# Kernel optimization log

Hardware: AMD Instinct MI355X
Metric: run time of the kernel (lower is better)

Reference implementation:

```python
import jax, jax.numpy as jnp
import numpy as np

B, T, D, H, E, R, M, HID, NB = 8, 832, 1024, 16, 16, 8, 16, 4096, 576
LORA_SCALE = 1.0 / R  # alpha / rank


def _ln(x, g, b, eps=1e-6):
    m = x.mean(-1, keepdims=True)
    v = ((x - m) ** 2).mean(-1, keepdims=True)
    return (x - m) / jnp.sqrt(v + eps) * g + b


def setup_inputs() -> dict:
    key = jax.random.key(0)
    ks = jax.random.split(key, 12)
    sd = 0.02
    return {
        's': jax.random.normal(ks[0], (B, T, D), jnp.float32),
        'attn_mask': jnp.zeros((1, 1, T, T), jnp.float32),
        'g1': jnp.ones((D,), jnp.float32),
        'b1': jnp.zeros((D,), jnp.float32),
        'w_qkv': jax.random.normal(ks[1], (D, 3 * D), jnp.float32) * sd,
        'b_qkv': jnp.zeros((3 * D,), jnp.float32),
        'w_proj': jax.random.normal(ks[2], (D, D), jnp.float32) * sd,
        'b_proj': jnp.zeros((D,), jnp.float32),
        'g2': jnp.ones((D,), jnp.float32),
        'b2': jnp.zeros((D,), jnp.float32),
        'w_fc1': jax.random.normal(ks[3], (D, HID), jnp.float32) * sd,
        'b_fc1': jnp.zeros((HID,), jnp.float32),
        'w_fc2': jax.random.normal(ks[4], (HID, D), jnp.float32) * sd,
        'b_fc2': jnp.zeros((D,), jnp.float32),
        'lora_A': jax.random.normal(ks[5], (E, D, R), jnp.float32) * sd,
        'lora_B': jax.random.normal(ks[6], (E, R, D), jnp.float32) * sd,
        'active_expert_indices': jnp.arange(E, dtype=jnp.int32),
        'num_backbone_tokens': NB,
    }


def reference(s, attn_mask, g1, b1, w_qkv, b_qkv, w_proj, b_proj,
              g2, b2, w_fc1, b_fc1, w_fc2, b_fc2, lora_A, lora_B,
              active_expert_indices, num_backbone_tokens):
    Bb, Tt, Dd = s.shape
    hd = Dd // H
    # --- shared attention ---
    x = _ln(s, g1, b1)
    qkv = (x @ w_qkv + b_qkv).reshape(Bb, Tt, 3, H, hd).transpose(2, 0, 3, 1, 4)
    q, k, v = qkv[0], qkv[1], qkv[2]  # [B,H,T,hd]
    scores = jnp.einsum('bhqd,bhkd->bhqk', q * (hd ** -0.5), k) + attn_mask
    p = jax.nn.softmax(scores, axis=-1)
    o = jnp.einsum('bhqk,bhkd->bhqd', p, v).transpose(0, 2, 1, 3).reshape(Bb, Tt, Dd)
    s = s + (o @ w_proj + b_proj)
    # --- shared MLP ---
    s_norm = _ln(s, g2, b2)
    shared = jax.nn.gelu(s_norm @ w_fc1 + b_fc1, approximate=False) @ w_fc2 + b_fc2
    # --- per-expert LoRA on expert token segment ---
    nb = num_backbone_tokens
    z = s_norm[:, nb:, :].reshape(Bb, -1, M, Dd)  # [B,K,M,D]
    Ak = lora_A[active_expert_indices]            # [K,D,R]
    Bk = lora_B[active_expert_indices]            # [K,R,D]
    down = jnp.einsum('bkmd,kdr->bkmr', z, Ak)
    up = jnp.einsum('bkmr,krd->bkmd', down, Bk) * LORA_SCALE
    shared = shared.at[:, nb:, :].add(up.reshape(Bb, -1, Dd))
    return s + shared
```

## Files before the change

### kernel.cpp

```cpp
#include <hip/hip_runtime.h>
#include <hip/hip_bf16.h>
#include <math.h>

typedef unsigned short u16;
typedef __attribute__((ext_vector_type(8))) short short8;
typedef __attribute__((ext_vector_type(4))) float f32x4;

constexpr int B_ = 8, T_ = 832, D_ = 1024, H_ = 16, HID_ = 4096, NB_ = 576;
constexpr int NT_ = B_ * T_;

__device__ inline u16 f2b(float f) {
    union { float f; unsigned u; } x{f};
    unsigned r = (x.u + 0x7FFFu + ((x.u >> 16) & 1u)) >> 16;
    return (u16)r;
}
__device__ inline float b2f(u16 b) {
    union { unsigned u; float f; } x; x.u = ((unsigned)b) << 16; return x.f;
}

__device__ inline float erf_inl(float x) {
    float ax = fabsf(x);
    float t = __frcp_rn(1.0f + 0.3275911f * ax);
    float p = 1.061405429f;
    p = p * t - 1.453152027f;
    p = p * t + 1.421413741f;
    p = p * t - 0.284496736f;
    p = p * t + 0.254829592f;
    p = p * t;
    float e = 1.0f - p * __expf(-ax * ax);
    return copysignf(e, x);
}

__device__ inline void gload_lds16(const void* g, void* l) {
    __builtin_amdgcn_global_load_lds((const __attribute__((address_space(1))) void*)g,
                                     (__attribute__((address_space(3))) void*)l, 16, 0, 0);
}

__global__ __launch_bounds__(256) void wtrans_kernel(const float* __restrict__ in,
                                                     u16* __restrict__ out, int K, int N) {
    __shared__ u16 tile[32][34];
    int n0 = blockIdx.x * 32, k0 = blockIdx.y * 32;
    int tx = threadIdx.x & 31, ty = threadIdx.x >> 5;
    for (int i = 0; i < 4; i++) {
        int k = k0 + ty + i * 8;
        tile[ty + i * 8][tx] = f2b(in[(size_t)k * N + n0 + tx]);
    }
    __syncthreads();
    for (int i = 0; i < 4; i++) {
        int n = n0 + ty + i * 8;
        out[(size_t)n * K + k0 + tx] = tile[tx][ty + i * 8];
    }
}

__global__ __launch_bounds__(256) void ln_kernel(const float* __restrict__ x,
                                                 const float* __restrict__ g,
                                                 const float* __restrict__ bt,
                                                 u16* __restrict__ out) {
    int row = blockIdx.x, tid = threadIdx.x;
    float4 v = ((const float4*)(x + (size_t)row * D_))[tid];
    float s = v.x + v.y + v.z + v.w;
    float q = v.x * v.x + v.y * v.y + v.z * v.z + v.w * v.w;
    for (int o = 1; o < 64; o <<= 1) { s += __shfl_xor(s, o); q += __shfl_xor(q, o); }
    __shared__ float red[4][2];
    if ((tid & 63) == 0) { red[tid >> 6][0] = s; red[tid >> 6][1] = q; }
    __syncthreads();
    s = red[0][0] + red[1][0] + red[2][0] + red[3][0];
    q = red[0][1] + red[1][1] + red[2][1] + red[3][1];
    float mean = s * (1.0f / D_);
    float var = q * (1.0f / D_) - mean * mean;
    float inv = rsqrtf(fmaxf(var, 0.f) + 1e-6f);
    float4 gv = ((const float4*)g)[tid];
    float4 bv = ((const float4*)bt)[tid];
    u16* orow = out + (size_t)row * D_ + tid * 4;
    orow[0] = f2b((v.x - mean) * inv * gv.x + bv.x);
    orow[1] = f2b((v.y - mean) * inv * gv.y + bv.y);
    orow[2] = f2b((v.z - mean) * inv * gv.z + bv.z);
    orow[3] = f2b((v.w - mean) * inv * gv.w + bv.w);
}

template<int BM, int BN, int WR, int WC, int MODE>
__global__ __launch_bounds__(WR * WC * 64, (WR * WC == 8) ? 2 : 3)
void gemm3(const u16* __restrict__ A, const u16* __restrict__ Bt,
           const float* __restrict__ bias, const float* __restrict__ resid,
           void* __restrict__ outp, int M, int N, int K) {
    constexpr int THREADS = WR * WC * 64;
    constexpr int MF = BM / WR / 16;
    constexpr int NF = BN / WC / 16;
    constexpr int NROWS = BM + BN;
    constexpr int CHUNKS = NROWS * 4 / THREADS;
    constexpr int LDSU = NROWS * 32;
    __shared__ u16 lds_[3 * LDSU];

    int tid = threadIdx.x, l = tid & 63, w = tid >> 6;
    int lrow = l & 15, lgrp = l >> 4;
    int wr = w / WC, wc = w % WC;

    int nwg = gridDim.x * gridDim.y;
    int bid = blockIdx.y * gridDim.x + blockIdx.x;
    int cpx = nwg >> 3;
    int swz = (bid & 7) * cpx + (bid >> 3);
    int bx = swz % gridDim.x, by = swz / gridDim.x;
    int m0 = by * BM, n0 = bx * BN;

    const u16* src[CHUNKS];
    int ldst[CHUNKS];
    for (int i = 0; i < CHUNKS; i++) {
        int c = i * THREADS + tid;
        int lc = (c & ~7) | ((c ^ (c >> 3)) & 7);
        int row = lc >> 2, colu = (lc & 3) * 8;
        src[i] = (row < BM) ? A + (size_t)(m0 + row) * K + colu
                            : Bt + (size_t)(n0 + row - BM) * K + colu;
        ldst[i] = c * 8;
    }

#define STAGE3(bufi, kt)                                                    \
    do {                                                                    \
        int kof = (kt) * 32;                                                \
        u16* bb = lds_ + (bufi) * LDSU;                                     \
        for (int i = 0; i < CHUNKS; i++) gload_lds16(src[i] + kof, bb + ldst[i]); \
    } while (0)

    f32x4 acc[MF][NF];
    for (int m = 0; m < MF; m++) for (int n = 0; n < NF; n++) acc[m][n] = (f32x4){0, 0, 0, 0};

    int aidx[MF], bidx[NF];
    for (int m = 0; m < MF; m++) {
        int row = wr * 64 + m * 16 + lrow;
        aidx[m] = (row * 32 + lgrp * 8) ^ (((row >> 1) & 7) << 3);
    }
    for (int n = 0; n < NF; n++) {
        int row = BM + wc * 64 + n * 16 + lrow;
        bidx[n] = (row * 32 + lgrp * 8) ^ (((row >> 1) & 7) << 3);
    }

    int nkt = K >> 5;
    STAGE3(0, 0);
    STAGE3(1, 1);
    if constexpr (CHUNKS == 3) asm volatile("s_waitcnt vmcnt(3)" ::: "memory");
    else                       asm volatile("s_waitcnt vmcnt(4)" ::: "memory");
    asm volatile("s_barrier" ::: "memory");

    int cur = 0;
    for (int t = 0; t < nkt; ++t) {
        int sb = cur + 2; if (sb >= 3) sb -= 3;
        if (t + 2 < nkt) STAGE3(sb, t + 2);

        const u16* bp = lds_ + cur * LDSU;
        short8 af[MF], bfr[NF];
        for (int m = 0; m < MF; m++) af[m] = *(const short8*)(bp + aidx[m]);
        for (int n = 0; n < NF; n++) bfr[n] = *(const short8*)(bp + bidx[n]);

        __builtin_amdgcn_s_setprio(1);
        for (int m = 0; m < MF; m++)
            for (int n = 0; n < NF; n++)
                acc[m][n] = __builtin_amdgcn_mfma_f32_16x16x32_bf16(af[m], bfr[n], acc[m][n], 0, 0, 0);
        __builtin_amdgcn_s_setprio(0);

        if (t + 2 < nkt) {
            if constexpr (CHUNKS == 3) asm volatile("s_waitcnt vmcnt(3)" ::: "memory");
            else                       asm volatile("s_waitcnt vmcnt(4)" ::: "memory");
        } else if (t + 1 < nkt) {
            asm volatile("s_waitcnt vmcnt(0)" ::: "memory");
        }
        asm volatile("s_barrier" ::: "memory");
        cur = cur + 1; if (cur == 3) cur = 0;
    }
#undef STAGE3

    for (int m = 0; m < MF; m++) {
        int rbase = m0 + wr * 64 + m * 16 + lgrp * 4;
        for (int n = 0; n < NF; n++) {
            int col = n0 + wc * 64 + n * 16 + lrow;
            float bv = bias[col];
            for (int j = 0; j < 4; j++) {
                int row = rbase + j;
                float v = acc[m][n][j] + bv;
                size_t off = (size_t)row * N + col;
                if constexpr (MODE == 0) {
                    ((u16*)outp)[off] = f2b(v);
                } else if constexpr (MODE == 1) {
                    ((float*)outp)[off] = v + resid[off];
                } else {
                    float gl = 0.5f * v * (1.0f + erf_inl(v * 0.70710678118654752f));
                    ((u16*)outp)[off] = f2b(gl);
                }
            }
        }
    }
}

__global__ __launch_bounds__(256) void vtrans_kernel(const u16* __restrict__ qkv,
                                                     u16* __restrict__ vt) {
    __shared__ u16 tile[32][66];
    int bh = blockIdx.y, b = bh >> 4, h = bh & 15;
    int t0 = blockIdx.x * 32;
    int dx = threadIdx.x & 63, ty = threadIdx.x >> 6;
    for (int i = 0; i < 8; i++) {
        int tt = ty * 8 + i;
        tile[tt][dx] = qkv[(size_t)(b * T_ + t0 + tt) * 3072 + 2048 + h * 64 + dx];
    }
    __syncthreads();
    int tx = threadIdx.x & 31, dy = threadIdx.x >> 5;
    for (int i = 0; i < 8; i++) {
        int d = dy * 8 + i;
        vt[((size_t)bh * 64 + d) * T_ + t0 + tx] = tile[tx][d];
    }
}

__global__ __launch_bounds__(512, 4) void attn_kernel(const u16* __restrict__ qkv,
                                                      const u16* __restrict__ vt,
                                                      const float* __restrict__ mask,
                                                      u16* __restrict__ obuf) {
    __shared__ u16 Ks[2][4096];
    __shared__ u16 Vs[2][4096];
    __shared__ u16 Ps[8][1024];
    int qt = blockIdx.x, bh = blockIdx.y, b = bh >> 4, h = bh & 15;
    int tid = threadIdx.x, w = tid >> 6, l = tid & 63;
    int lrow = l & 15, lgrp = l >> 4;

    int qrow = qt * 128 + w * 16 + lrow;
    int qrc = qrow < T_ ? qrow : T_ - 1;
    const u16* qp = qkv + (size_t)(b * T_ + qrc) * 3072 + h * 64 + lgrp * 8;
    short8 aq0, aq1;
    {
        short8 r0 = *(const short8*)qp;
        short8 r1 = *(const short8*)(qp + 32);
        for (int i = 0; i < 8; i++) {
            aq0[i] = (short)f2b(b2f((u16)r0[i]) * 0.125f);
            aq1[i] = (short)f2b(b2f((u16)r1[i]) * 0.125f);
        }
    }

    int tq0 = qt * 128 + w * 16 + lgrp * 4;
    bool qvalid = tq0 < T_;
    const float* mrowp[4];
#pragma unroll
    for (int j = 0; j < 4; j++) {
        int tq = tq0 + j; if (tq >= T_) tq = T_ - 1;
        mrowp[j] = mask + (size_t)tq * T_;
    }

    float m_r[4], l_r[4];
    f32x4 oacc[4];
    for (int j = 0; j < 4; j++) { m_r[j] = -1e30f; l_r[j] = 0.f; }
    for (int n = 0; n < 4; n++) oacc[n] = (f32x4){0, 0, 0, 0};

    int srow = tid >> 3, sp = tid & 7;
    int se = (sp ^ (srow & 7)) * 8;
    const u16* kbase = qkv + (size_t)b * T_ * 3072 + 1024 + h * 64;
    const u16* vbase = vt + (size_t)bh * 64 * T_;

#define STAGE_KV(buf, kk0)                                                        \
    do {                                                                          \
        gload_lds16(kbase + (size_t)((kk0) + srow) * 3072 + se, &Ks[buf][w * 512]); \
        gload_lds16(vbase + (size_t)srow * T_ + (kk0) + se, &Vs[buf][w * 512]);     \
    } while (0)

    float mc[16], mn[16];
    STAGE_KV(0, 0);
#pragma unroll
    for (int j = 0; j < 4; j++)
#pragma unroll
        for (int c = 0; c < 4; c++)
            mc[j * 4 + c] = mrowp[j][c * 16 + lrow];
    __syncthreads();

    int cur = 0;
    u16* Pw = Ps[w];
    int swl = lrow & 7;
    int slot0 = (lgrp ^ swl) * 8, slot1 = ((lgrp + 4) ^ swl) * 8;

    for (int kt = 0; kt < 13; ++kt) {
        int kk0 = kt * 64;
        if (kt < 12) {
            STAGE_KV(cur ^ 1, kk0 + 64);
#pragma unroll
            for (int j = 0; j < 4; j++)
#pragma unroll
                for (int c = 0; c < 4; c++)
                    mn[j * 4 + c] = mrowp[j][kk0 + 64 + c * 16 + lrow];
        }

        f32x4 sc[4];
        for (int c = 0; c < 4; c++) sc[c] = (f32x4){0, 0, 0, 0};
        const u16* Kb = Ks[cur];
        __builtin_amdgcn_s_setprio(1);
        for (int c = 0; c < 4; c++) {
            const u16* krow = Kb + (c * 16 + lrow) * 64;
            short8 bk0 = *(const short8*)(krow + slot0);
            short8 bk1 = *(const short8*)(krow + slot1);
            sc[c] = __builtin_amdgcn_mfma_f32_16x16x32_bf16(aq0, bk0, sc[c], 0, 0, 0);
            sc[c] = __builtin_amdgcn_mfma_f32_16x16x32_bf16(aq1, bk1, sc[c], 0, 0, 0);
        }
        __builtin_amdgcn_s_setprio(0);

        int lo3 = lrow & 7, hi = lrow >> 3;
#pragma unroll
        for (int j = 0; j < 4; j++) {
            float s0 = sc[0][j] + mc[j * 4 + 0];
            float s1 = sc[1][j] + mc[j * 4 + 1];
            float s2 = sc[2][j] + mc[j * 4 + 2];
            float s3 = sc[3][j] + mc[j * 4 + 3];
            float mx = fmaxf(fmaxf(s0, s1), fmaxf(s2, s3));
            mx = fmaxf(mx, __shfl_xor(mx, 1));
            mx = fmaxf(mx, __shfl_xor(mx, 2));
            mx = fmaxf(mx, __shfl_xor(mx, 4));
            mx = fmaxf(mx, __shfl_xor(mx, 8));
            float mnew = fmaxf(m_r[j], mx);
            float scf = __expf(m_r[j] - mnew);
            float p0 = __expf(s0 - mnew), p1 = __expf(s1 - mnew);
            float p2 = __expf(s2 - mnew), p3 = __expf(s3 - mnew);
            float ps = (p0 + p1) + (p2 + p3);
            ps += __shfl_xor(ps, 1); ps += __shfl_xor(ps, 2);
            ps += __shfl_xor(ps, 4); ps += __shfl_xor(ps, 8);
            l_r[j] = l_r[j] * scf + ps;
            m_r[j] = mnew;
            for (int n = 0; n < 4; n++) oacc[n][j] *= scf;
            int row_p = lgrp * 4 + j, swp = row_p & 7;
            u16* pr = Pw + row_p * 64;
            pr[((hi ^ swp) * 8) + lo3]       = f2b(p0);
            pr[(((2 + hi) ^ swp) * 8) + lo3] = f2b(p1);
            pr[(((4 + hi) ^ swp) * 8) + lo3] = f2b(p2);
            pr[(((6 + hi) ^ swp) * 8) + lo3] = f2b(p3);
        }

        short8 ap0 = *(const short8*)&Pw[lrow * 64 + slot0];
        short8 ap1 = *(const short8*)&Pw[lrow * 64 + slot1];
        const u16* Vb = Vs[cur];
        __builtin_amdgcn_s_setprio(1);
        for (int n = 0; n < 4; n++) {
            const u16* vrow = Vb + (n * 16 + lrow) * 64;
            short8 bv0 = *(const short8*)(vrow + slot0);
            short8 bv1 = *(const short8*)(vrow + slot1);
            oacc[n] = __builtin_amdgcn_mfma_f32_16x16x32_bf16(ap0, bv0, oacc[n], 0, 0, 0);
            oacc[n] = __builtin_amdgcn_mfma_f32_16x16x32_bf16(ap1, bv1, oacc[n], 0, 0, 0);
        }
        __builtin_amdgcn_s_setprio(0);

        __syncthreads();
#pragma unroll
        for (int i = 0; i < 16; i++) mc[i] = mn[i];
        cur ^= 1;
    }
#undef STAGE_KV

    if (qvalid) {
        for (int j = 0; j < 4; j++) {
            float inv = 1.0f / l_r[j];
            int t = tq0 + j;
            for (int n = 0; n < 4; n++)
                obuf[(size_t)(b * T_ + t) * 1024 + h * 64 + n * 16 + lrow] = f2b(oacc[n][j] * inv);
        }
    }
}

__global__ __launch_bounds__(256) void lora_kernel(const u16* __restrict__ snorm,
                                                   const float* __restrict__ lA,
                                                   const float* __restrict__ lB,
                                                   const int* __restrict__ idx,
                                                   float* __restrict__ outp) {
    __shared__ float down[16][8];
    int blk = blockIdx.x, b = blk >> 4, kk = blk & 15;
    int e = idx[kk];
    int tok0 = b * T_ + NB_ + kk * 16;
    int tid = threadIdx.x;
    if (tid < 128) {
        int m = tid >> 3, r = tid & 7;
        const u16* z = snorm + (size_t)(tok0 + m) * D_;
        const float* Ae = lA + (size_t)e * D_ * 8 + r;
        float acc = 0.f;
        for (int d = 0; d < D_; ++d) acc += b2f(z[d]) * Ae[(size_t)d * 8];
        down[m][r] = acc;
    }
    __syncthreads();
    for (int ci = 0; ci < 4; ci++) {
        int col = tid + ci * 256;
        float br[8];
        for (int r = 0; r < 8; r++) br[r] = lB[((size_t)e * 8 + r) * D_ + col];
        for (int m = 0; m < 16; m++) {
            float acc = 0.f;
            for (int r = 0; r < 8; r++) acc += down[m][r] * br[r];
            outp[(size_t)(tok0 + m) * D_ + col] += acc * 0.125f;
        }
    }
}

extern "C" void kernel_launch(void* const* d_in, const int* in_sizes, int n_in,
                              void* d_out, int out_size, void* d_ws, size_t ws_size,
                              hipStream_t stream) {
    const float* s      = (const float*)d_in[0];
    const float* mask   = (const float*)d_in[1];
    const float* g1     = (const float*)d_in[2];
    const float* b1     = (const float*)d_in[3];
    const float* w_qkv  = (const float*)d_in[4];
    const float* b_qkv  = (const float*)d_in[5];
    const float* w_proj = (const float*)d_in[6];
    const float* b_proj = (const float*)d_in[7];
    const float* g2     = (const float*)d_in[8];
    const float* b2     = (const float*)d_in[9];
    const float* w_fc1  = (const float*)d_in[10];
    const float* b_fc1  = (const float*)d_in[11];
    const float* w_fc2  = (const float*)d_in[12];
    const float* b_fc2  = (const float*)d_in[13];
    const float* lA     = (const float*)d_in[14];
    const float* lB     = (const float*)d_in[15];
    const int*   eidx   = (const int*)d_in[16];
    float* out = (float*)d_out;
    char* ws = (char*)d_ws;

    u16*   wqkvT = (u16*)(ws + 0);
    u16*   wprojT= (u16*)(ws + 6291456);
    u16*   wfc1T = (u16*)(ws + 8388608);
    u16*   wfc2T = (u16*)(ws + 16777216);
    float* s1    = (float*)(ws + 25165824);
    u16*   xln   = (u16*)(ws + 52428800);
    u16*   vt    = (u16*)(ws + 66060288);
    u16*   qkv   = (u16*)(ws + 79691776);
    u16*   h     = (u16*)(ws + 66060288);

    wtrans_kernel<<<dim3(3072 / 32, 1024 / 32), 256, 0, stream>>>(w_qkv, wqkvT, 1024, 3072);
    wtrans_kernel<<<dim3(1024 / 32, 1024 / 32), 256, 0, stream>>>(w_proj, wprojT, 1024, 1024);
    wtrans_kernel<<<dim3(4096 / 32, 1024 / 32), 256, 0, stream>>>(w_fc1, wfc1T, 1024, 4096);
    wtrans_kernel<<<dim3(1024 / 32, 4096 / 32), 256, 0, stream>>>(w_fc2, wfc2T, 4096, 1024);

    ln_kernel<<<NT_, 256, 0, stream>>>(s, g1, b1, xln);
    gemm3<128, 256, 2, 4, 0><<<dim3(3072 / 256, NT_ / 128), 512, 0, stream>>>(xln, wqkvT, b_qkv, nullptr, qkv, NT_, 3072, 1024);
    vtrans_kernel<<<dim3(26, 128), 256, 0, stream>>>(qkv, vt);
    attn_kernel<<<dim3(7, 128), 512, 0, stream>>>(qkv, vt, mask, xln);
    gemm3<128, 128, 2, 2, 1><<<dim3(1024 / 128, NT_ / 128), 256, 0, stream>>>(xln, wprojT, b_proj, s, s1, NT_, 1024, 1024);
    ln_kernel<<<NT_, 256, 0, stream>>>(s1, g2, b2, xln);
    gemm3<128, 256, 2, 4, 2><<<dim3(4096 / 256, NT_ / 128), 512, 0, stream>>>(xln, wfc1T, b_fc1, nullptr, h, NT_, 4096, 1024);
    gemm3<128, 128, 2, 2, 1><<<dim3(1024 / 128, NT_ / 128), 256, 0, stream>>>(h, wfc2T, b_fc2, s1, out, NT_, 1024, 4096);
    lora_kernel<<<128, 256, 0, stream>>>(xln, lA, lB, eidx, out);
}
```

Baseline: 431.3 us.

## Add 256x256 double-buffered GEMM kernel for QKV and FC1 projections

Introduces a new gemm4 kernel with 256x256 output tiles, 8 waves each computing 128x64, two LDS buffers with XOR-swizzled direct global-to-LDS loads, XCD-aware block swizzling and MFMA priority hints. It replaces the triple-buffered 128x256 gemm3 for the QKV and FC1 GEMMs. The larger tile is meant to raise arithmetic intensity and cut redundant global loads. In exchange each thread holds 128 accumulator registers, there are fewer workgroups (312 for QKV), and there is less pipelining depth.

```diff
diff --git a/kernel.cpp b/kernel.cpp
--- a/kernel.cpp
+++ b/kernel.cpp
@@ -76,6 +76,103 @@
     orow[1] = f2b((v.y - mean) * inv * gv.y + bv.y);
     orow[2] = f2b((v.z - mean) * inv * gv.z + bv.z);
     orow[3] = f2b((v.w - mean) * inv * gv.w + bv.w);
+}
+
+template<int MODE>
+__global__ __launch_bounds__(512, 2)
+void gemm4(const u16* __restrict__ A, const u16* __restrict__ Bt,
+           const float* __restrict__ bias, void* __restrict__ outp,
+           int M, int N, int K) {
+    __shared__ u16 lds4[2][16384];
+    int tid = threadIdx.x, l = tid & 63, w = tid >> 6;
+    int lrow = l & 15, lgrp = l >> 4;
+    int wr = w >> 2, wc = w & 3;
+
+    int nwg = gridDim.x * gridDim.y;
+    int bid = blockIdx.y * gridDim.x + blockIdx.x;
+    int cpx = nwg >> 3;
+    int swz = (bid & 7) * cpx + (bid >> 3);
+    int bx = swz % gridDim.x, by = swz / gridDim.x;
+    int m0 = by * 256, n0 = bx * 256;
+
+    const u16* src[4];
+    int ldst[4];
+    for (int i = 0; i < 2; i++) {
+        int c = i * 512 + tid;
+        int row = c >> 2, s = c & 3;
+        int col = (s ^ (row & 3)) * 8;
+        src[i]     = A  + (size_t)(m0 + row) * K + col;
+        ldst[i]    = c * 8;
+        src[i + 2] = Bt + (size_t)(n0 + row) * K + col;
+        ldst[i + 2] = 8192 + c * 8;
+    }
+
+#define STAGE4(cb, t)                                                       \
+    do {                                                                    \
+        u16* bb = &lds4[cb][0];                                             \
+        int ko = (t) * 32;                                                  \
+        for (int i = 0; i < 4; i++) gload_lds16(src[i] + ko, bb + ldst[i]); \
+    } while (0)
+
+    f32x4 acc[8][4];
+    for (int m = 0; m < 8; m++) for (int n = 0; n < 4; n++) acc[m][n] = (f32x4){0, 0, 0, 0};
+
+    int sl = (lgrp ^ (lrow & 3)) * 8;
+    int aidx[8], bidx[4];
+    for (int m = 0; m < 8; m++) {
+        int row = wr * 128 + (m >> 2) * 64 + (m & 3) * 16 + lrow;
+        aidx[m] = row * 32 + sl;
+    }
+    for (int n = 0; n < 4; n++) {
+        int row = wc * 64 + n * 16 + lrow;
+        bidx[n] = 8192 + row * 32 + sl;
+    }
+
+    int nkt = K >> 5;
+    STAGE4(0, 0);
+    asm volatile("s_waitcnt vmcnt(0)" ::: "memory");
+    asm volatile("s_barrier" ::: "memory");
+
+    for (int t = 0; t < nkt; ++t) {
+        int cb = t & 1;
+        if (t + 1 < nkt) STAGE4(cb ^ 1, t + 1);
+        const u16* bp = &lds4[cb][0];
+        short8 bf[4];
+        for (int n = 0; n < 4; n++) bf[n] = *(const short8*)(bp + bidx[n]);
+        for (int hm = 0; hm < 2; hm++) {
+            short8 af[4];
+            for (int mi = 0; mi < 4; mi++) af[mi] = *(const short8*)(bp + aidx[hm * 4 + mi]);
+            __builtin_amdgcn_s_setprio(1);
+            for (int mi = 0; mi < 4; mi++)
+                for (int n = 0; n < 4; n++)
+                    acc[hm * 4 + mi][n] =
+                        __builtin_amdgcn_mfma_f32_16x16x32_bf16(af[mi], bf[n], acc[hm * 4 + mi][n], 0, 0, 0);
+            __builtin_amdgcn_s_setprio(0);
+        }
+        if (t + 1 < nkt) {
+            asm volatile("s_waitcnt vmcnt(0)" ::: "memory");
+            asm volatile("s_barrier" ::: "memory");
+        }
+    }
+#undef STAGE4
+
+    for (int m = 0; m < 8; m++) {
+        int rbase = m0 + wr * 128 + (m >> 2) * 64 + (m & 3) * 16 + lgrp * 4;
+        for (int n = 0; n < 4; n++) {
+            int col = n0 + wc * 64 + n * 16 + lrow;
+            float bv = bias[col];
+            for (int j = 0; j < 4; j++) {
+                float v = acc[m][n][j] + bv;
+                size_t off = (size_t)(rbase + j) * N + col;
+                if constexpr (MODE == 0) {
+                    ((u16*)outp)[off] = f2b(v);
+                } else {
+                    float gl = 0.5f * v * (1.0f + erf_inl(v * 0.70710678118654752f));
+                    ((u16*)outp)[off] = f2b(gl);
+                }
+            }
+        }
+    }
 }
 
 template<int BM, int BN, int WR, int WC, int MODE>
@@ -424,12 +521,12 @@
     wtrans_kernel<<<dim3(1024 / 32, 4096 / 32), 256, 0, stream>>>(w_fc2, wfc2T, 4096, 1024);
 
     ln_kernel<<<NT_, 256, 0, stream>>>(s, g1, b1, xln);
-    gemm3<128, 256, 2, 4, 0><<<dim3(3072 / 256, NT_ / 128), 512, 0, stream>>>(xln, wqkvT, b_qkv, nullptr, qkv, NT_, 3072, 1024);
+    gemm4<0><<<dim3(3072 / 256, NT_ / 256), 512, 0, stream>>>(xln, wqkvT, b_qkv, qkv, NT_, 3072, 1024);
     vtrans_kernel<<<dim3(26, 128), 256, 0, stream>>>(qkv, vt);
     attn_kernel<<<dim3(7, 128), 512, 0, stream>>>(qkv, vt, mask, xln);
     gemm3<128, 128, 2, 2, 1><<<dim3(1024 / 128, NT_ / 128), 256, 0, stream>>>(xln, wprojT, b_proj, s, s1, NT_, 1024, 1024);
     ln_kernel<<<NT_, 256, 0, stream>>>(s1, g2, b2, xln);
-    gemm3<128, 256, 2, 4, 2><<<dim3(4096 / 256, NT_ / 128), 512, 0, stream>>>(xln, wfc1T, b_fc1, nullptr, h, NT_, 4096, 1024);
+    gemm4<2><<<dim3(4096 / 256, NT_ / 256), 512, 0, stream>>>(xln, wfc1T, b_fc1, h, NT_, 4096, 1024);
     gemm3<128, 128, 2, 2, 1><<<dim3(1024 / 128, NT_ / 128), 256, 0, stream>>>(h, wfc2T, b_fc2, s1, out, NT_, 1024, 4096);
     lora_kernel<<<128, 256, 0, stream>>>(xln, lA, lB, eidx, out);
 }
```

Result: slower. 477.6 us (+10.7%).
